# Optimization experiments

Hardware: AMD Instinct MI355X
Metric: run time of the kernel (lower is better)

Reference implementation:

```python
import jax, jax.numpy as jnp
import numpy as np
import math

DIM = 768
HEADS = 12
HEAD_DIM = DIM // HEADS
SCALE_PARAM_INIT = 1.0 / math.sqrt(DIM)  # Scale(scale=1/sqrt(dim), init=1.0)


def cosine_norm(x, eps=1e-6):
    norm = jnp.maximum(jnp.linalg.norm(x, axis=-1, keepdims=True), eps)
    return x / norm


def setup_inputs() -> dict:
    key = jax.random.key(0)
    ks = jax.random.split(key, 6)
    B, N = 8, 1024
    x = jax.random.normal(ks[0], (B, N, DIM), dtype=jnp.float32)
    # torch nn.Linear weights are [out, in]; y = x @ W^T
    std = 1.0 / math.sqrt(DIM)
    Wq = jax.random.uniform(ks[1], (DIM, DIM), jnp.float32, -std, std)
    Wk = jax.random.uniform(ks[2], (DIM, DIM), jnp.float32, -std, std)
    Wv = jax.random.uniform(ks[3], (DIM, DIM), jnp.float32, -std, std)
    Wo = jax.random.uniform(ks[4], (DIM, DIM), jnp.float32, -std, std)
    # Scale param s: ones * scale, perturbed slightly for generality
    s_qk = SCALE_PARAM_INIT * (1.0 + 0.1 * jax.random.normal(ks[5], (HEADS, HEAD_DIM), jnp.float32))
    return {"x": x, "Wq": Wq, "Wk": Wk, "Wv": Wv, "Wo": Wo, "s_qk": s_qk}


def reference(x, Wq, Wk, Wv, Wo, s_qk):
    B, N, _ = x.shape
    # projections (torch Linear: x @ W^T)
    q = (x @ Wq.T).reshape(B, N, HEADS, HEAD_DIM)
    k = (x @ Wk.T).reshape(B, N, HEADS, HEAD_DIM)
    v = (x @ Wv.T).reshape(B, N, HEADS, HEAD_DIM)
    # effective scale = s * (init / scale)
    s_eff = s_qk * (1.0 / SCALE_PARAM_INIT)  # [H, D]
    q = cosine_norm(q) * s_eff  # broadcast over [B, N, H, D]
    k = cosine_norm(k) * s_eff
    scale = HEAD_DIM ** 0.5  # note: multiplies logits (nGPT-style)
    # [B, H, N, N]
    logits = jnp.einsum('bqhd,bkhd->bhqk', q, k) * scale
    attn = jax.nn.softmax(logits, axis=-1)
    out = jnp.einsum('bhqk,bkhd->bqhd', attn, v).reshape(B, N, HEADS * HEAD_DIM)
    return out @ Wo.T
```

## Files before the change

kernel.cpp:

```cpp
#include <hip/hip_runtime.h>
#include <hip/hip_bf16.h>
#include <math.h>

#define NDIM 768
#define NHEADS 12
#define HD 64
#define SEQ 1024
#define BATCH 8
#define MROWS (BATCH * SEQ)
#define SQRT_DIM 27.712812921102035f
#define LOG2E 1.4426950408889634f

typedef unsigned short u16;
typedef unsigned int u32;
typedef __attribute__((ext_vector_type(8))) short short8;
typedef __attribute__((ext_vector_type(4))) short bf16x4;
typedef __attribute__((ext_vector_type(4))) float f32x4;
typedef __attribute__((ext_vector_type(16))) float f32x16;

#define MFMA16(a, b, c) __builtin_amdgcn_mfma_f32_16x16x32_bf16(a, b, c, 0, 0, 0)
#define MFMA32(a, b, c) __builtin_amdgcn_mfma_f32_32x32x16_bf16(a, b, c, 0, 0, 0)

#if __has_builtin(__builtin_amdgcn_exp2f)
#define EXP2(x) __builtin_amdgcn_exp2f(x)
#else
#define EXP2(x) exp2f(x)
#endif

__device__ inline u16 f2bf(float f) {
    __hip_bfloat16 h = __float2bfloat16(f);
    return *reinterpret_cast<u16*>(&h);
}

__device__ inline u32 rne_pack(float a, float b) {
    u32 ua = __builtin_bit_cast(u32, a), ub = __builtin_bit_cast(u32, b);
    ua = (ua + 0x7fffu + ((ua >> 16) & 1u)) >> 16;
    ub = (ub + 0x7fffu + ((ub >> 16) & 1u)) >> 16;
    return (ub << 16) | ua;
}

__device__ inline void gl2lds16(const void* g, void* l) {
    __builtin_amdgcn_global_load_lds((const __attribute__((address_space(1))) void*)g,
                                     (__attribute__((address_space(3))) void*)l, 16, 0, 0);
}

__global__ __launch_bounds__(256) void castall(const float* __restrict__ x,
                                               const float* __restrict__ Wq,
                                               const float* __restrict__ Wk,
                                               const float* __restrict__ Wv,
                                               const float* __restrict__ Wo,
                                               u16* __restrict__ xb,
                                               u16* __restrict__ Wqkv,
                                               u16* __restrict__ Wob) {
    const int WB = (NDIM * NDIM) / 1024;
    int blk = blockIdx.x;
    const float* s;
    u16* d;
    int base;
    if (blk < 6144) {
        s = x; d = xb; base = blk * 1024;
    } else {
        int wsel = (blk - 6144) / WB, r = (blk - 6144) % WB;
        base = r * 1024;
        if (wsel == 0)      { s = Wq; d = Wqkv; }
        else if (wsel == 1) { s = Wk; d = Wqkv + NDIM * NDIM; }
        else if (wsel == 2) { s = Wv; d = Wqkv + 2 * NDIM * NDIM; }
        else                { s = Wo; d = Wob; }
    }
    int i = base + threadIdx.x * 4;
    float4 v = *(const float4*)(s + i);
    uint2 o = make_uint2(rne_pack(v.x, v.y), rne_pack(v.z, v.w));
    *(uint2*)(d + i) = o;
}

template <int EPI>
__global__ __launch_bounds__(256) void gemm_bf16(const u16* __restrict__ A,
                                                 const u16* __restrict__ B,
                                                 void* __restrict__ C, int N,
                                                 const float* __restrict__ s_qk,
                                                 u16* __restrict__ Qdst,
                                                 u16* __restrict__ Kdst,
                                                 int NX) {
    constexpr int K = NDIM;
    constexpr int NKT = K / 32;
    __shared__ __align__(16) u16 As[2][4096];
    __shared__ __align__(16) u16 Bs[2][4096];
    const int t = threadIdx.x;
    const int wave = t >> 6, lane = t & 63;
    const int quad = lane >> 4, l16 = lane & 15;
    const int wx = (wave & 1) * 64, wy = (wave >> 1) * 64;
    const int blk = blockIdx.x;
    const int xcd = blk & 7, local = blk >> 3;
    const int bm = (xcd * 8 + local / NX) * 128;
    const int bn = (local % NX) * 128;

    f32x4 acc[4][4];
#pragma unroll
    for (int i = 0; i < 4; ++i)
#pragma unroll
        for (int j = 0; j < 4; ++j) acc[i][j] = (f32x4){0.f, 0.f, 0.f, 0.f};

    const int srl = lane >> 2;
    const int skc = (lane & 3) ^ ((lane >> 3) & 3);
    auto stage = [&](int k0, int bsel) {
#pragma unroll
        for (int it = 0; it < 2; ++it) {
            const int cb = it * 256 + wave * 64;
            const int row = (cb >> 6) * 16 + srl;
            gl2lds16(A + (size_t)(bm + row) * K + k0 + skc * 8,
                     (char*)As[bsel] + cb * 16);
            gl2lds16(B + (size_t)(bn + row) * K + k0 + skc * 8,
                     (char*)Bs[bsel] + cb * 16);
        }
    };
    const int fxor = (l16 >> 1) & 3;

    stage(0, 0);
#pragma unroll
    for (int kt = 0; kt < NKT; ++kt) {
        __syncthreads();
        if (kt + 1 < NKT) stage((kt + 1) * 32, (kt + 1) & 1);
        const int b = kt & 1;
        short8 af[4], bfr[4];
#pragma unroll
        for (int i = 0; i < 4; ++i)
            af[i] = *(const short8*)&As[b][
                ((((wy >> 4) + i) * 64 + l16 * 4 + (quad ^ fxor)) * 8)];
#pragma unroll
        for (int j = 0; j < 4; ++j)
            bfr[j] = *(const short8*)&Bs[b][
                ((((wx >> 4) + j) * 64 + l16 * 4 + (quad ^ fxor)) * 8)];
#pragma unroll
        for (int i = 0; i < 4; ++i)
#pragma unroll
            for (int j = 0; j < 4; ++j) acc[i][j] = MFMA16(af[i], bfr[j], acc[i][j]);
    }

    if constexpr (EPI == 0) {
#pragma unroll
        for (int i = 0; i < 4; ++i)
#pragma unroll
            for (int j = 0; j < 4; ++j)
#pragma unroll
                for (int r = 0; r < 4; ++r) {
                    const int row = bm + wy + i * 16 + quad * 4 + r;
                    const int col = bn + wx + j * 16 + l16;
                    ((float*)C)[(size_t)row * N + col] = acc[i][j][r];
                }
    } else {
        const int cg = (bn + wx) >> 6;
        if (cg >= 2 * NHEADS) {
            const int h = cg - 2 * NHEADS;
#pragma unroll
            for (int i = 0; i < 4; ++i)
#pragma unroll
                for (int j = 0; j < 4; ++j)
#pragma unroll
                    for (int r = 0; r < 4; ++r) {
                        const int row = bm + wy + i * 16 + quad * 4 + r;
                        const int dd = j * 16 + l16;
                        const int b = row >> 10, n = row & 1023;
                        ((u16*)C)[(((size_t)(b * NHEADS + h) * HD + dd) << 10) + n] =
                            f2bf(acc[i][j][r]);
                    }
        } else {
            const bool isq = cg < NHEADS;
            const int h = isq ? cg : cg - NHEADS;
            u16* dst = isq ? Qdst : Kdst;
            const float ex = isq ? 8.f * LOG2E : 1.f;
            float sq[4];
#pragma unroll
            for (int j = 0; j < 4; ++j)
                sq[j] = s_qk[h * HD + j * 16 + l16] * SQRT_DIM * ex;
#pragma unroll
            for (int i = 0; i < 4; ++i)
#pragma unroll
                for (int r = 0; r < 4; ++r) {
                    float ss = 0.f;
#pragma unroll
                    for (int j = 0; j < 4; ++j) ss += acc[i][j][r] * acc[i][j][r];
                    ss += __shfl_xor(ss, 1, 64);
                    ss += __shfl_xor(ss, 2, 64);
                    ss += __shfl_xor(ss, 4, 64);
                    ss += __shfl_xor(ss, 8, 64);
                    float inv = 1.f / fmaxf(sqrtf(ss), 1e-6f);
                    const int row = bm + wy + i * 16 + quad * 4 + r;
                    const int b = row >> 10, tok = row & 1023;
                    u16* o = dst + ((size_t)(b * NHEADS + h) * SEQ + tok) * HD;
#pragma unroll
                    for (int j = 0; j < 4; ++j)
                        o[j * 16 + l16] = f2bf(acc[i][j][r] * sq[j] * inv);
                }
        }
    }
}

__global__ __launch_bounds__(256) void attn_mfma(const u16* __restrict__ Qh,
                                                 const u16* __restrict__ Kh,
                                                 const u16* __restrict__ Vt,
                                                 u16* __restrict__ AO) {
    __shared__ __align__(16) u16 Ks[512 * 8];
    __shared__ __align__(16) u16 Vs[512 * 8];
    __shared__ __align__(16) u16 Ps[4 * 32 * 64];

    const int t = threadIdx.x;
    const int wave = t >> 6, lane = t & 63;
    const int l31 = lane & 31, half = lane >> 5;
    const int b = blockIdx.z, h = blockIdx.y, q0 = blockIdx.x * 128;
    const int bh = b * NHEADS + h;
    const u16* Kb = Kh + (size_t)bh * SEQ * HD;
    const u16* Vb = Vt + (size_t)bh * HD * SEQ;
    const int qb = q0 + wave * 32;
    const int pbase = wave * 2048 + l31 * 64;
    const int sw = (l31 & 15);

    short8 qf[4];
#pragma unroll
    for (int tt = 0; tt < 4; ++tt)
        qf[tt] = *(const short8*)(Qh + ((size_t)bh * SEQ + qb + l31) * HD +
                                  tt * 16 + half * 8);

    f32x16 o[2];
#pragma unroll
    for (int dt = 0; dt < 2; ++dt)
#pragma unroll
        for (int r = 0; r < 16; ++r) o[dt][r] = 0.f;
    float lp = 0.f;

    const int arl = lane >> 3;
    const int acc8 = (lane & 7) ^ arl;
    const int fx8 = l31 & 7;

    for (int j0 = 0; j0 < SEQ; j0 += 64) {
        __syncthreads();
#pragma unroll
        for (int it = 0; it < 2; ++it) {
            const int cb = it * 256 + wave * 64;
            const int r0 = (cb >> 6) * 8 + arl;
            gl2lds16(Kb + (size_t)(j0 + r0) * HD + acc8 * 8, (char*)Ks + cb * 16);
            gl2lds16(Vb + (size_t)r0 * SEQ + j0 + acc8 * 8, (char*)Vs + cb * 16);
        }
        asm volatile("s_waitcnt vmcnt(0)" ::: "memory");
        __syncthreads();

#pragma unroll
        for (int kt = 0; kt < 2; ++kt) {
            f32x16 sa;
#pragma unroll
            for (int r = 0; r < 16; ++r) sa[r] = 0.f;
#pragma unroll
            for (int tt = 0; tt < 4; ++tt) {
                short8 kf = *(const short8*)&Ks[
                    (((kt * 4 + (l31 >> 3)) * 64) + fx8 * 8 +
                     ((2 * tt + half) ^ fx8)) * 8];
                sa = MFMA32(kf, qf[tt], sa);
            }
#pragma unroll
            for (int rg = 0; rg < 4; ++rg) {
                float p0 = EXP2(sa[rg * 4 + 0]);
                float p1 = EXP2(sa[rg * 4 + 1]);
                float p2 = EXP2(sa[rg * 4 + 2]);
                float p3 = EXP2(sa[rg * 4 + 3]);
                lp += (p0 + p1) + (p2 + p3);
                uint2 pk = make_uint2(rne_pack(p0, p1), rne_pack(p2, p3));
                const int u = kt * 8 + rg * 2 + half;
                *(uint2*)&Ps[pbase + (u ^ sw) * 4] = pk;
            }
        }

#pragma unroll
        for (int k2 = 0; k2 < 4; ++k2) {
            const int u0 = k2 * 4 + half * 2;
            bf16x4 lo = *(const bf16x4*)&Ps[pbase + ((u0 + 0) ^ sw) * 4];
            bf16x4 hi = *(const bf16x4*)&Ps[pbase + ((u0 + 1) ^ sw) * 4];
            short8 pf = __builtin_shufflevector(lo, hi, 0, 1, 2, 3, 4, 5, 6, 7);
#pragma unroll
            for (int dt = 0; dt < 2; ++dt) {
                short8 vf = *(const short8*)&Vs[
                    (((dt * 4 + (l31 >> 3)) * 64) + fx8 * 8 +
                     ((2 * k2 + half) ^ fx8)) * 8];
                o[dt] = MFMA32(vf, pf, o[dt]);
            }
        }
    }

    const float invl = 1.f / (lp + __shfl_xor(lp, 32, 64));
    u16* ob = AO + (size_t)(b * SEQ + qb + l31) * NDIM + h * HD;
#pragma unroll
    for (int dt = 0; dt < 2; ++dt)
#pragma unroll
        for (int rg = 0; rg < 4; ++rg) {
            bf16x4 ok = {(short)f2bf(o[dt][rg * 4 + 0] * invl),
                         (short)f2bf(o[dt][rg * 4 + 1] * invl),
                         (short)f2bf(o[dt][rg * 4 + 2] * invl),
                         (short)f2bf(o[dt][rg * 4 + 3] * invl)};
            *(bf16x4*)(ob + dt * 32 + rg * 8 + half * 4) = ok;
        }
}

extern "C" void kernel_launch(void* const* d_in, const int* in_sizes, int n_in,
                              void* d_out, int out_size, void* d_ws, size_t ws_size,
                              hipStream_t stream) {
    const float* x    = (const float*)d_in[0];
    const float* Wq   = (const float*)d_in[1];
    const float* Wk   = (const float*)d_in[2];
    const float* Wv   = (const float*)d_in[3];
    const float* Wo   = (const float*)d_in[4];
    const float* s_qk = (const float*)d_in[5];
    float* out = (float*)d_out;

    char* w = (char*)d_ws;
    const size_t TE = (size_t)MROWS * NDIM;
    u16* xb   = (u16*)w;                    w += TE * 2;
    u16* Wqkv = (u16*)w;                    w += (size_t)3 * NDIM * NDIM * 2;
    u16* Wob  = (u16*)w;                    w += (size_t)NDIM * NDIM * 2;
    u16* Qh   = (u16*)w;                    w += TE * 2;
    u16* Kh   = (u16*)w;                    w += TE * 2;
    u16* Vt   = (u16*)w;                    w += TE * 2;
    u16* ao   = (u16*)w;

    castall<<<6144 + 4 * 576, 256, 0, stream>>>(x, Wq, Wk, Wv, Wo, xb, Wqkv, Wob);

    gemm_bf16<2><<<18 * 64, 256, 0, stream>>>(
        xb, Wqkv, (void*)Vt, 2304, s_qk, Qh, Kh, 18);

    attn_mfma<<<dim3(SEQ / 128, NHEADS, BATCH), 256, 0, stream>>>(Qh, Kh, Vt, ao);

    gemm_bf16<0><<<6 * 64, 256, 0, stream>>>(
        ao, Wob, out, NDIM, nullptr, nullptr, nullptr, 6);
}
```

Baseline: 198.7 us.

## Load GEMM B operand directly to registers and shrink output-projection M tile

```diff
diff --git a/kernel.cpp b/kernel.cpp
--- a/kernel.cpp
+++ b/kernel.cpp
@@ -73,7 +73,7 @@
     *(uint2*)(d + i) = o;
 }
 
-template <int EPI>
+template <int EPI, int TM>
 __global__ __launch_bounds__(256) void gemm_bf16(const u16* __restrict__ A,
                                                  const u16* __restrict__ B,
                                                  void* __restrict__ C, int N,
@@ -83,62 +83,70 @@
                                                  int NX) {
     constexpr int K = NDIM;
     constexpr int NKT = K / 32;
-    __shared__ __align__(16) u16 As[2][4096];
-    __shared__ __align__(16) u16 Bs[2][4096];
+    constexpr int MI = TM / 32;
+    __shared__ __align__(16) u16 As[2][TM * 32];
     const int t = threadIdx.x;
     const int wave = t >> 6, lane = t & 63;
     const int quad = lane >> 4, l16 = lane & 15;
-    const int wx = (wave & 1) * 64, wy = (wave >> 1) * 64;
+    const int wx = (wave & 1) * 64, wy = (wave >> 1) * (TM / 2);
     const int blk = blockIdx.x;
     const int xcd = blk & 7, local = blk >> 3;
-    const int bm = (xcd * 8 + local / NX) * 128;
+    constexpr int MT_PER_XCD = (MROWS / TM) / 8;
+    const int bm = (xcd * MT_PER_XCD + local / NX) * TM;
     const int bn = (local % NX) * 128;
 
-    f32x4 acc[4][4];
-#pragma unroll
-    for (int i = 0; i < 4; ++i)
+    f32x4 acc[MI][4];
+#pragma unroll
+    for (int i = 0; i < MI; ++i)
 #pragma unroll
         for (int j = 0; j < 4; ++j) acc[i][j] = (f32x4){0.f, 0.f, 0.f, 0.f};
 
     const int srl = lane >> 2;
     const int skc = (lane & 3) ^ ((lane >> 3) & 3);
-    auto stage = [&](int k0, int bsel) {
-#pragma unroll
-        for (int it = 0; it < 2; ++it) {
+    auto stageA = [&](int k0, int bsel) {
+#pragma unroll
+        for (int it = 0; it < TM / 64; ++it) {
             const int cb = it * 256 + wave * 64;
             const int row = (cb >> 6) * 16 + srl;
             gl2lds16(A + (size_t)(bm + row) * K + k0 + skc * 8,
                      (char*)As[bsel] + cb * 16);
-            gl2lds16(B + (size_t)(bn + row) * K + k0 + skc * 8,
-                     (char*)Bs[bsel] + cb * 16);
-        }
+        }
+    };
+    auto loadB = [&](int k0, short8* bf) {
+#pragma unroll
+        for (int j = 0; j < 4; ++j)
+            bf[j] = *(const short8*)(B + (size_t)(bn + wx + j * 16 + l16) * K +
+                                     k0 + quad * 8);
     };
     const int fxor = (l16 >> 1) & 3;
 
-    stage(0, 0);
+    short8 bcur[4], bnext[4];
+    stageA(0, 0);
+    loadB(0, bcur);
 #pragma unroll
     for (int kt = 0; kt < NKT; ++kt) {
         __syncthreads();
-        if (kt + 1 < NKT) stage((kt + 1) * 32, (kt + 1) & 1);
+        if (kt + 1 < NKT) {
+            stageA((kt + 1) * 32, (kt + 1) & 1);
+            loadB((kt + 1) * 32, bnext);
+        }
         const int b = kt & 1;
-        short8 af[4], bfr[4];
-#pragma unroll
-        for (int i = 0; i < 4; ++i)
+        short8 af[MI];
+#pragma unroll
+        for (int i = 0; i < MI; ++i)
             af[i] = *(const short8*)&As[b][
                 ((((wy >> 4) + i) * 64 + l16 * 4 + (quad ^ fxor)) * 8)];
 #pragma unroll
-        for (int j = 0; j < 4; ++j)
-            bfr[j] = *(const short8*)&Bs[b][
-                ((((wx >> 4) + j) * 64 + l16 * 4 + (quad ^ fxor)) * 8)];
-#pragma unroll
-        for (int i = 0; i < 4; ++i)
-#pragma unroll
-            for (int j = 0; j < 4; ++j) acc[i][j] = MFMA16(af[i], bfr[j], acc[i][j]);
+        for (int i = 0; i < MI; ++i)
+#pragma unroll
+            for (int j = 0; j < 4; ++j) acc[i][j] = MFMA16(af[i], bcur[j], acc[i][j]);
+#pragma unroll
+        for (int j = 0; j < 4; ++j) bcur[j] = bnext[j];
     }
 
     if constexpr (EPI == 0) {
 #pragma unroll
-        for (int i = 0; i < 4; ++i)
+        for (int i = 0; i < MI; ++i)
 #pragma unroll
             for (int j = 0; j < 4; ++j)
 #pragma unroll
@@ -152,7 +160,7 @@
         if (cg >= 2 * NHEADS) {
             const int h = cg - 2 * NHEADS;
 #pragma unroll
-            for (int i = 0; i < 4; ++i)
+            for (int i = 0; i < MI; ++i)
 #pragma unroll
                 for (int j = 0; j < 4; ++j)
 #pragma unroll
@@ -173,7 +181,7 @@
             for (int j = 0; j < 4; ++j)
                 sq[j] = s_qk[h * HD + j * 16 + l16] * SQRT_DIM * ex;
 #pragma unroll
-            for (int i = 0; i < 4; ++i)
+            for (int i = 0; i < MI; ++i)
 #pragma unroll
                 for (int r = 0; r < 4; ++r) {
                     float ss = 0.f;
@@ -321,11 +329,11 @@
 
     castall<<<6144 + 4 * 576, 256, 0, stream>>>(x, Wq, Wk, Wv, Wo, xb, Wqkv, Wob);
 
-    gemm_bf16<2><<<18 * 64, 256, 0, stream>>>(
+    gemm_bf16<2, 128><<<18 * 64, 256, 0, stream>>>(
         xb, Wqkv, (void*)Vt, 2304, s_qk, Qh, Kh, 18);
 
     attn_mfma<<<dim3(SEQ / 128, NHEADS, BATCH), 256, 0, stream>>>(Qh, Kh, Vt, ao);
 
-    gemm_bf16<0><<<6 * 64, 256, 0, stream>>>(
+    gemm_bf16<0, 64><<<6 * 128, 256, 0, stream>>>(
         ao, Wob, out, NDIM, nullptr, nullptr, nullptr, 6);
 }
```

Result: slower. 243.3 us (+22.4%).
